# Kernel tuning notes

Hardware: AMD Instinct MI355X
Metric: run time of the kernel (lower is better)

Reference implementation:

```python
import jax, jax.numpy as jnp
import numpy as np

NUM_HEADS = 8
EPS = 1e-6


def _edge_boost(x, density_weight):
    # x: [B, C, H, W] -> boost: [B, H*W] (per-query additive bias)
    B, C, H, W = x.shape
    sx = jnp.array([[-1., 0., 1.], [-2., 0., 2.], [-1., 0., 1.]], dtype=x.dtype)
    sy = jnp.array([[-1., -2., -1.], [0., 0., 0.], [1., 2., 1.]], dtype=x.dtype)
    feat_mean = x.mean(axis=1, keepdims=True)            # [B,1,H,W]
    kern = jnp.stack([sx, sy])[:, None]                  # [2,1,3,3] (OIHW)
    g = jax.lax.conv_general_dilated(
        feat_mean, kern, window_strides=(1, 1), padding='SAME',
        dimension_numbers=('NCHW', 'OIHW', 'NCHW'))     # [B,2,H,W]
    edge = jnp.sqrt(g[:, 0] ** 2 + g[:, 1] ** 2 + EPS)   # [B,H,W]
    return density_weight * jnp.log1p(edge.reshape(B, H * W))


def setup_inputs() -> dict:
    key = jax.random.key(0)
    k1, k2, k3 = jax.random.split(key, 3)
    B, C, H, W = 2, 256, 56, 56
    x = jax.random.normal(k1, (B, C, H, W), dtype=jnp.float32)
    Wqkv = jax.random.normal(k2, (3 * C, C), dtype=jnp.float32) * 0.02
    Wproj = jax.random.normal(k3, (C, C), dtype=jnp.float32) * 0.02
    bproj = jnp.zeros((C,), dtype=jnp.float32)
    density_weight = jnp.float32(1.0)
    return {"x": x, "Wqkv": Wqkv, "Wproj": Wproj, "bproj": bproj,
            "density_weight": density_weight}


def reference(x, Wqkv, Wproj, bproj, density_weight):
    B, C, H, W = x.shape
    h = NUM_HEADS
    d = C // h
    N = H * W
    scale = d ** -0.5

    x_flat = x.reshape(B, C, N).transpose(0, 2, 1)        # [B,N,C]
    qkv = x_flat @ Wqkv.T                                 # [B,N,3C]
    qkv = qkv.reshape(B, N, 3, h, d).transpose(2, 0, 3, 1, 4)  # [3,B,h,N,d]
    q, k, v = qkv[0], qkv[1], qkv[2]

    attn = jnp.einsum('bhqd,bhkd->bhqk', q, k) * scale    # [B,h,N,N]
    boost = _edge_boost(x, density_weight)                # [B,N]
    attn = attn + boost[:, None, :, None]                 # per-query bias, bcast over heads/keys
    attn = jax.nn.softmax(attn, axis=-1)
    # dropout is identity in eval mode

    out = jnp.einsum('bhqk,bhkd->bhqd', attn, v)          # [B,h,N,d]
    out = out.transpose(0, 2, 1, 3).reshape(B, N, C)      # [B,N,C]
    out = out @ Wproj.T + bproj
    return out.transpose(0, 2, 1).reshape(B, C, H, W)
```

## Files before the change

kernel.cpp:

```cpp
#include <hip/hip_runtime.h>
#include <hip/hip_bf16.h>
#include <math.h>

#define NQ    3136
#define CDIM  256
#define HEADS 8
#define NT    49


typedef __attribute__((ext_vector_type(8))) short short8;
typedef __attribute__((ext_vector_type(4))) float f32x4;

__device__ __forceinline__ short f2bf(float f) {
    union { float f; unsigned u; } v; v.f = f;
    unsigned r = v.u + 0x7fff + ((v.u >> 16) & 1);
    return (short)(r >> 16);
}

__device__ __forceinline__ unsigned pk_bf16(float a, float b) {
    unsigned r;
    asm("v_cvt_pk_bf16_f32 %0, %1, %2" : "=v"(r) : "v"(a), "v"(b));
    return r;
}

#define SCALE_L2E 0.25503487523f

__global__ __launch_bounds__(256) void prep(const float* __restrict__ x,
                                            const float* __restrict__ Wq,
                                            const float* __restrict__ Wp,
                                            short* __restrict__ xT,
                                            short* __restrict__ Wb,
                                            short* __restrict__ Wpb) {
    const int bx = blockIdx.x;
    const int t  = threadIdx.x;
    if (bx == 52) {
        const int wp   = blockIdx.y + 4 * blockIdx.z;
        const int base = wp * 8192 + t * 4;
        #pragma unroll
        for (int i = 0; i < 8; ++i) {
            float4 v = *(const float4*)(Wp + base + i * 1024);
            uint2 o = { pk_bf16(v.x, v.y), pk_bf16(v.z, v.w) };
            *(uint2*)(Wpb + base + i * 1024) = o;
        }
        return;
    }
    if (bx >= 49) {
        const int wb   = (bx - 49) + 3 * (blockIdx.y + 4 * blockIdx.z);
        const int base = wb * 8192 + t * 4;
        #pragma unroll
        for (int i = 0; i < 8; ++i) {
            float4 v = *(const float4*)(Wq + base + i * 1024);
            uint2 o = { pk_bf16(v.x, v.y), pk_bf16(v.z, v.w) };
            *(uint2*)(Wb + base + i * 1024) = o;
        }
        return;
    }
    __shared__ short lt[64][72];
    const int b = blockIdx.z, cb = blockIdx.y, nb = bx;
    const float* xb = x + (size_t)b * CDIM * NQ + (size_t)(cb * 64) * NQ + nb * 64;
    #pragma unroll
    for (int it = 0; it < 4; ++it) {
        const int cc = (t >> 4) + 16 * it;
        const int nn = (t & 15) * 4;
        float4 v = *(const float4*)(xb + (size_t)cc * NQ + nn);
        lt[nn + 0][cc] = f2bf(v.x);
        lt[nn + 1][cc] = f2bf(v.y);
        lt[nn + 2][cc] = f2bf(v.z);
        lt[nn + 3][cc] = f2bf(v.w);
    }
    __syncthreads();
    const int n2 = t >> 2, c2 = (t & 3) * 16;
    short* dst = xT + ((size_t)b * NQ + nb * 64 + n2) * CDIM + cb * 64 + c2;
    *(uint4*)dst       = *(const uint4*)&lt[n2][c2];
    *(uint4*)(dst + 8) = *(const uint4*)&lt[n2][c2 + 8];
}

__global__ __launch_bounds__(256) void qkv_mfma(const short* __restrict__ xT,
                                                const short* __restrict__ Wb,
                                                short* __restrict__ Qs,
                                                short* __restrict__ Kb,
                                                short* __restrict__ Vt) {
    __shared__ short xs[64][40];
    __shared__ short wsm[64][40];
    __shared__ short eps[64][72];
    const int nb = blockIdx.x, jb = blockIdx.y, b = blockIdx.z;
    const int n0 = nb * 64, j0 = jb * 64;
    const int t = threadIdx.x;
    const int lane = t & 63, w = t >> 6, g = lane >> 4, ql = lane & 15;
    const int srow = t >> 2, sc = (t & 3) * 8;

    const short* xsrc = xT + ((size_t)b * NQ + n0 + srow) * CDIM + sc;
    const short* wsrc = Wb + (size_t)(j0 + srow) * CDIM + sc;

    short8 xr = *(const short8*)(xsrc);
    short8 wr = *(const short8*)(wsrc);

    f32x4 acc[4] = {};
    for (int c0 = 0; c0 < 256; c0 += 32) {
        *(short8*)&xs[srow][sc]  = xr;
        *(short8*)&wsm[srow][sc] = wr;
        __syncthreads();
        if (c0 + 32 < 256) {
            xr = *(const short8*)(xsrc + c0 + 32);
            wr = *(const short8*)(wsrc + c0 + 32);
        }
        short8 bf = *(const short8*)&wsm[16 * w + ql][8 * g];
        #pragma unroll
        for (int r = 0; r < 4; ++r) {
            short8 af = *(const short8*)&xs[16 * r + ql][8 * g];
            acc[r] = __builtin_amdgcn_mfma_f32_16x16x32_bf16(af, bf, acc[r], 0, 0, 0);
        }
        __syncthreads();
    }

    const int sect = jb >> 2;
    const int hb   = (jb & 3) * 2;
    const int jloc = 16 * w + ql;

    if (sect < 2) {
        const float sc2 = (sect == 0) ? SCALE_L2E : 1.0f;
        #pragma unroll
        for (int r = 0; r < 4; ++r)
            #pragma unroll
            for (int i = 0; i < 4; ++i)
                eps[16 * r + 4 * g + i][jloc] = f2bf(acc[r][i] * sc2);
        __syncthreads();
        short* dstb = (sect == 0) ? Qs : Kb;
        const int n2 = t >> 2, jc = (t & 3) * 16;
        const int head = hb + (jc >> 5), d0 = jc & 31;
        short* dst = dstb + ((size_t)(b * 8 + head) * NQ + n0 + n2) * 32 + d0;
        *(uint4*)dst       = *(const uint4*)&eps[n2][jc];
        *(uint4*)(dst + 8) = *(const uint4*)&eps[n2][jc + 8];
    } else {
        #pragma unroll
        for (int r = 0; r < 4; ++r)
            #pragma unroll
            for (int i = 0; i < 4; ++i)
                eps[jloc][16 * r + 4 * g + i] = f2bf(acc[r][i]);
        __syncthreads();
        const int jl = t >> 2, nc = (t & 3) * 16;
        short* dst = Vt + ((size_t)(b * 8 + hb + (jl >> 5)) * 32 + (jl & 31)) * NQ + n0 + nc;
        *(uint4*)dst       = *(const uint4*)&eps[jl][nc];
        *(uint4*)(dst + 8) = *(const uint4*)&eps[jl][nc + 8];
    }
}

__global__ __launch_bounds__(256) void attn_mfma(const short* __restrict__ Qs,
                                                 const short* __restrict__ Kb,
                                                 const short* __restrict__ Vt,
                                                 short* __restrict__ Ob) {
    __shared__ __align__(16) short vts[2][2][32][72];
    __shared__ __align__(16) short pq[4][32][72];

    const int bid = blockIdx.x;
    const int xcd = bid & 7;
    const int ii  = bid >> 3;
    const int bh  = xcd * 2 + (ii & 1);
    const int q0  = (ii >> 1) * 64;

    const int t    = threadIdx.x;
    const int lane = t & 63;
    const int w    = t >> 6;
    const int g    = lane >> 4;
    const int ql   = lane & 15;
    const int qg   = w & 1, half = w >> 1;
    const int qbase = q0 + 32 * qg;

    const short* Qh = Qs + (size_t)bh * NQ * 32;
    const short* Kh = Kb + (size_t)bh * NQ * 32;
    const short* Vh = Vt + (size_t)bh * 32 * NQ;

    const short8 qfA = *(const short8*)(Qh + (size_t)(qbase + ql) * 32 + 8 * g);
    const short8 qfB = *(const short8*)(Qh + (size_t)(qbase + 16 + ql) * 32 + 8 * g);

    const short* kp = Kh + (size_t)ql * 32 + 8 * g;

    const int vrow = (t & 127) >> 2;
    const int vu   = (t & 3) * 16;

    float lA = 0.f, lB = 0.f;
    f32x4 otA0 = {0,0,0,0}, otA1 = {0,0,0,0};
    f32x4 otB0 = {0,0,0,0}, otB1 = {0,0,0,0};

    short8 vr0 = *(const short8*)(Vh + (size_t)vrow * NQ + half * 64 + vu);
    short8 vr1 = *(const short8*)(Vh + (size_t)vrow * NQ + half * 64 + vu + 8);
    short8 kf0 = *(const short8*)(kp + (size_t)(half * 64 +  0) * 32);
    short8 kf1 = *(const short8*)(kp + (size_t)(half * 64 + 16) * 32);
    short8 kf2 = *(const short8*)(kp + (size_t)(half * 64 + 32) * 32);
    short8 kf3 = *(const short8*)(kp + (size_t)(half * 64 + 48) * 32);
    *(short8*)&vts[half][0][vrow][vu]     = vr0;
    *(short8*)&vts[half][0][vrow][vu + 8] = vr1;
    __syncthreads();

    int buf = 0;
    for (int i = 0; i < 25; ++i) {
        const int cur = 2 * i + half;
        const int nxt = cur + 2;
        if (nxt < NT) {
            vr0 = *(const short8*)(Vh + (size_t)vrow * NQ + nxt * 64 + vu);
            vr1 = *(const short8*)(Vh + (size_t)vrow * NQ + nxt * 64 + vu + 8);
        }

        if (cur < NT) {
            f32x4 stA[4], stB[4];
            stA[0] = __builtin_amdgcn_mfma_f32_16x16x32_bf16(kf0, qfA, (f32x4){0,0,0,0}, 0, 0, 0);
            stB[0] = __builtin_amdgcn_mfma_f32_16x16x32_bf16(kf0, qfB, (f32x4){0,0,0,0}, 0, 0, 0);
            stA[1] = __builtin_amdgcn_mfma_f32_16x16x32_bf16(kf1, qfA, (f32x4){0,0,0,0}, 0, 0, 0);
            stB[1] = __builtin_amdgcn_mfma_f32_16x16x32_bf16(kf1, qfB, (f32x4){0,0,0,0}, 0, 0, 0);
            stA[2] = __builtin_amdgcn_mfma_f32_16x16x32_bf16(kf2, qfA, (f32x4){0,0,0,0}, 0, 0, 0);
            stB[2] = __builtin_amdgcn_mfma_f32_16x16x32_bf16(kf2, qfB, (f32x4){0,0,0,0}, 0, 0, 0);
            stA[3] = __builtin_amdgcn_mfma_f32_16x16x32_bf16(kf3, qfA, (f32x4){0,0,0,0}, 0, 0, 0);
            stB[3] = __builtin_amdgcn_mfma_f32_16x16x32_bf16(kf3, qfB, (f32x4){0,0,0,0}, 0, 0, 0);

            if (nxt < NT) {
                const int kn = nxt * 64;
                kf0 = *(const short8*)(kp + (size_t)(kn +  0) * 32);
                kf1 = *(const short8*)(kp + (size_t)(kn + 16) * 32);
                kf2 = *(const short8*)(kp + (size_t)(kn + 32) * 32);
                kf3 = *(const short8*)(kp + (size_t)(kn + 48) * 32);
            }

            float pA[16], pB[16];
            #pragma unroll
            for (int c = 0; c < 4; ++c)
                #pragma unroll
                for (int e = 0; e < 4; ++e) {
                    pA[4 * c + e] = __builtin_amdgcn_exp2f(stA[c][e]);
                    pB[4 * c + e] = __builtin_amdgcn_exp2f(stB[c][e]);
                }
            float sA = 0.f, sB = 0.f;
            #pragma unroll
            for (int e = 0; e < 16; ++e) { sA += pA[e]; sB += pB[e]; }
            lA += sA; lB += sB;

            #pragma unroll
            for (int c = 0; c < 4; ++c) {
                uint2 va_ = { pk_bf16(pA[4 * c + 0], pA[4 * c + 1]),
                              pk_bf16(pA[4 * c + 2], pA[4 * c + 3]) };
                *(uint2*)&pq[w][ql][16 * c + 4 * g] = va_;
                uint2 vb_ = { pk_bf16(pB[4 * c + 0], pB[4 * c + 1]),
                              pk_bf16(pB[4 * c + 2], pB[4 * c + 3]) };
                *(uint2*)&pq[w][16 + ql][16 * c + 4 * g] = vb_;
            }
            asm volatile("s_waitcnt lgkmcnt(0)" ::: "memory");

            short8 pbA0 = *(const short8*)&pq[w][ql][8 * g];
            short8 pbA1 = *(const short8*)&pq[w][ql][32 + 8 * g];
            short8 pbB0 = *(const short8*)&pq[w][16 + ql][8 * g];
            short8 pbB1 = *(const short8*)&pq[w][16 + ql][32 + 8 * g];
            short8 va00 = *(const short8*)&vts[half][buf][ql][8 * g];
            short8 va01 = *(const short8*)&vts[half][buf][ql][32 + 8 * g];
            short8 va10 = *(const short8*)&vts[half][buf][16 + ql][8 * g];
            short8 va11 = *(const short8*)&vts[half][buf][16 + ql][32 + 8 * g];

            otA0 = __builtin_amdgcn_mfma_f32_16x16x32_bf16(va00, pbA0, otA0, 0, 0, 0);
            otA0 = __builtin_amdgcn_mfma_f32_16x16x32_bf16(va01, pbA1, otA0, 0, 0, 0);
            otA1 = __builtin_amdgcn_mfma_f32_16x16x32_bf16(va10, pbA0, otA1, 0, 0, 0);
            otA1 = __builtin_amdgcn_mfma_f32_16x16x32_bf16(va11, pbA1, otA1, 0, 0, 0);
            otB0 = __builtin_amdgcn_mfma_f32_16x16x32_bf16(va00, pbB0, otB0, 0, 0, 0);
            otB0 = __builtin_amdgcn_mfma_f32_16x16x32_bf16(va01, pbB1, otB0, 0, 0, 0);
            otB1 = __builtin_amdgcn_mfma_f32_16x16x32_bf16(va10, pbB0, otB1, 0, 0, 0);
            otB1 = __builtin_amdgcn_mfma_f32_16x16x32_bf16(va11, pbB1, otB1, 0, 0, 0);
        }

        if (nxt < NT) {
            *(short8*)&vts[half][buf ^ 1][vrow][vu]     = vr0;
            *(short8*)&vts[half][buf ^ 1][vrow][vu + 8] = vr1;
        }
        __syncthreads();
        buf ^= 1;
    }

    lA += __shfl_xor(lA, 16); lA += __shfl_xor(lA, 32);
    lB += __shfl_xor(lB, 16); lB += __shfl_xor(lB, 32);

    float* mrg = (float*)&pq[0][0][0];
    if (half == 1) {
        float* pp = mrg + ((size_t)qg * 64 + lane) * 20;
        *(f32x4*)(pp + 0)  = otA0;
        *(f32x4*)(pp + 4)  = otA1;
        *(f32x4*)(pp + 8)  = otB0;
        *(f32x4*)(pp + 12) = otB1;
        pp[16] = lA; pp[17] = lB;
    }
    __syncthreads();
    if (half == 0) {
        const float* pp = mrg + ((size_t)qg * 64 + lane) * 20;
        f32x4 a0 = *(const f32x4*)(pp + 0);
        f32x4 a1 = *(const f32x4*)(pp + 4);
        f32x4 b0 = *(const f32x4*)(pp + 8);
        f32x4 b1 = *(const f32x4*)(pp + 12);
        const float invA = 1.f / (lA + pp[16]);
        const float invB = 1.f / (lB + pp[17]);
        const int b = bh >> 3, h = bh & 7;
        short* orowA = Ob + ((size_t)b * NQ + qbase + ql) * CDIM + h * 32;
        short* orowB = Ob + ((size_t)b * NQ + qbase + 16 + ql) * CDIM + h * 32;
        uint2 wA0 = { pk_bf16((otA0[0]+a0[0])*invA, (otA0[1]+a0[1])*invA),
                      pk_bf16((otA0[2]+a0[2])*invA, (otA0[3]+a0[3])*invA) };
        uint2 wA1 = { pk_bf16((otA1[0]+a1[0])*invA, (otA1[1]+a1[1])*invA),
                      pk_bf16((otA1[2]+a1[2])*invA, (otA1[3]+a1[3])*invA) };
        uint2 wB0 = { pk_bf16((otB0[0]+b0[0])*invB, (otB0[1]+b0[1])*invB),
                      pk_bf16((otB0[2]+b0[2])*invB, (otB0[3]+b0[3])*invB) };
        uint2 wB1 = { pk_bf16((otB1[0]+b1[0])*invB, (otB1[1]+b1[1])*invB),
                      pk_bf16((otB1[2]+b1[2])*invB, (otB1[3]+b1[3])*invB) };
        *(uint2*)(orowA + 4 * g)      = wA0;
        *(uint2*)(orowA + 16 + 4 * g) = wA1;
        *(uint2*)(orowB + 4 * g)      = wB0;
        *(uint2*)(orowB + 16 + 4 * g) = wB1;
    }
}

__global__ __launch_bounds__(256) void proj_mfma(const short* __restrict__ Ob,
                                                 const short* __restrict__ Wpb,
                                                 const float* __restrict__ bias,
                                                 float* __restrict__ out) {
    __shared__ short xs[32][40];
    __shared__ short wsm[64][40];
    __shared__ float eps[64][36];
    const int n0  = blockIdx.x * 32;
    const int co0 = blockIdx.y * 64;
    const int b   = blockIdx.z;
    const int t   = threadIdx.x;
    const int lane = t & 63, w = t >> 6, g = lane >> 4, ql = lane & 15;
    const int arow = (t & 127) >> 2, ac = (t & 3) * 8;
    const int brow = t >> 2,          bc = (t & 3) * 8;

    const short* asrc = Ob + ((size_t)b * NQ + n0 + arow) * CDIM + ac;
    const short* wsrc = Wpb + (size_t)(co0 + brow) * CDIM + bc;

    short8 ar = {};
    if (t < 128) ar = *(const short8*)(asrc);
    short8 wr = *(const short8*)(wsrc);

    f32x4 acc0 = {}, acc1 = {};
    for (int c0 = 0; c0 < 256; c0 += 32) {
        if (t < 128) *(short8*)&xs[arow][ac] = ar;
        *(short8*)&wsm[brow][bc] = wr;
        __syncthreads();
        if (c0 + 32 < 256) {
            if (t < 128) ar = *(const short8*)(asrc + c0 + 32);
            wr = *(const short8*)(wsrc + c0 + 32);
        }
        short8 bfr = *(const short8*)&wsm[16 * w + ql][8 * g];
        short8 af0 = *(const short8*)&xs[ql][8 * g];
        short8 af1 = *(const short8*)&xs[16 + ql][8 * g];
        acc0 = __builtin_amdgcn_mfma_f32_16x16x32_bf16(af0, bfr, acc0, 0, 0, 0);
        acc1 = __builtin_amdgcn_mfma_f32_16x16x32_bf16(af1, bfr, acc1, 0, 0, 0);
        __syncthreads();
    }

    const int jl = 16 * w + ql;
    const float bb = bias[co0 + jl];
    *(float4*)&eps[jl][4 * g]      = make_float4(acc0[0] + bb, acc0[1] + bb,
                                                 acc0[2] + bb, acc0[3] + bb);
    *(float4*)&eps[jl][16 + 4 * g] = make_float4(acc1[0] + bb, acc1[1] + bb,
                                                 acc1[2] + bb, acc1[3] + bb);
    __syncthreads();

    const int row = t >> 2, seg = (t & 3) * 8;
    float* outp = out + ((size_t)b * CDIM + co0 + row) * NQ + n0 + seg;
    *(float4*)(outp)     = *(const float4*)&eps[row][seg];
    *(float4*)(outp + 4) = *(const float4*)&eps[row][seg + 4];
}

extern "C" void kernel_launch(void* const* d_in, const int* in_sizes, int n_in,
                              void* d_out, int out_size, void* d_ws, size_t ws_size,
                              hipStream_t stream) {
    const float* x     = (const float*)d_in[0];
    const float* Wqkv  = (const float*)d_in[1];
    const float* Wproj = (const float*)d_in[2];
    const float* bproj = (const float*)d_in[3];
    float* out = (float*)d_out;

    short* xT  = (short*)d_ws;
    short* Wb  = xT + (size_t)2 * NQ * CDIM;
    short* Wpb = Wb + (size_t)768 * CDIM;
    short* Qs  = Wpb + (size_t)CDIM * CDIM;
    short* Kb  = Qs + (size_t)16 * NQ * 32;
    short* Vt  = Kb + (size_t)16 * NQ * 32;
    short* Ob  = Vt + (size_t)16 * NQ * 32;

    prep<<<dim3(53, 4, 2), 256, 0, stream>>>(x, Wqkv, Wproj, xT, Wb, Wpb);
    qkv_mfma<<<dim3(49, 12, 2), 256, 0, stream>>>(xT, Wb, Qs, Kb, Vt);
    attn_mfma<<<dim3(784, 1, 1), 256, 0, stream>>>(Qs, Kb, Vt, Ob);
    proj_mfma<<<dim3(98, 4, 2), 256, 0, stream>>>(Ob, Wpb, bproj, out);
}
```

Measured before the change: 78.10 us.

## Halve attention query tile per block and load K fragments in-loop

Each attention block now handles 32 queries instead of 64, with each wave computing one 16-query group, and the grid doubles to 1568 blocks. K fragments are loaded at the top of each iteration instead of being prefetched one step ahead. This cuts per-wave registers and LDS, which can raise occupancy and parallelism. The cost is halved K/V reuse per block, so global K/V traffic doubles, and K load latency is no longer hidden.

```diff
diff --git a/kernel.cpp b/kernel.cpp
--- a/kernel.cpp
+++ b/kernel.cpp
@@ -150,13 +150,13 @@
                                                  const short* __restrict__ Vt,
                                                  short* __restrict__ Ob) {
     __shared__ __align__(16) short vts[2][2][32][72];
-    __shared__ __align__(16) short pq[4][32][72];
+    __shared__ __align__(16) short pq[4][16][72];
 
     const int bid = blockIdx.x;
     const int xcd = bid & 7;
     const int ii  = bid >> 3;
     const int bh  = xcd * 2 + (ii & 1);
-    const int q0  = (ii >> 1) * 64;
+    const int q0  = (ii >> 1) * 32;
 
     const int t    = threadIdx.x;
     const int lane = t & 63;
@@ -164,30 +164,24 @@
     const int g    = lane >> 4;
     const int ql   = lane & 15;
     const int qg   = w & 1, half = w >> 1;
-    const int qbase = q0 + 32 * qg;
+    const int qbase = q0 + 16 * qg;
 
     const short* Qh = Qs + (size_t)bh * NQ * 32;
     const short* Kh = Kb + (size_t)bh * NQ * 32;
     const short* Vh = Vt + (size_t)bh * 32 * NQ;
 
-    const short8 qfA = *(const short8*)(Qh + (size_t)(qbase + ql) * 32 + 8 * g);
-    const short8 qfB = *(const short8*)(Qh + (size_t)(qbase + 16 + ql) * 32 + 8 * g);
+    const short8 qf = *(const short8*)(Qh + (size_t)(qbase + ql) * 32 + 8 * g);
 
     const short* kp = Kh + (size_t)ql * 32 + 8 * g;
 
     const int vrow = (t & 127) >> 2;
     const int vu   = (t & 3) * 16;
 
-    float lA = 0.f, lB = 0.f;
-    f32x4 otA0 = {0,0,0,0}, otA1 = {0,0,0,0};
-    f32x4 otB0 = {0,0,0,0}, otB1 = {0,0,0,0};
+    float l = 0.f;
+    f32x4 ot0 = {0,0,0,0}, ot1 = {0,0,0,0};
 
     short8 vr0 = *(const short8*)(Vh + (size_t)vrow * NQ + half * 64 + vu);
     short8 vr1 = *(const short8*)(Vh + (size_t)vrow * NQ + half * 64 + vu + 8);
-    short8 kf0 = *(const short8*)(kp + (size_t)(half * 64 +  0) * 32);
-    short8 kf1 = *(const short8*)(kp + (size_t)(half * 64 + 16) * 32);
-    short8 kf2 = *(const short8*)(kp + (size_t)(half * 64 + 32) * 32);
-    short8 kf3 = *(const short8*)(kp + (size_t)(half * 64 + 48) * 32);
     *(short8*)&vts[half][0][vrow][vu]     = vr0;
     *(short8*)&vts[half][0][vrow][vu + 8] = vr1;
     __syncthreads();
@@ -202,65 +196,48 @@
         }
 
         if (cur < NT) {
-            f32x4 stA[4], stB[4];
-            stA[0] = __builtin_amdgcn_mfma_f32_16x16x32_bf16(kf0, qfA, (f32x4){0,0,0,0}, 0, 0, 0);
-            stB[0] = __builtin_amdgcn_mfma_f32_16x16x32_bf16(kf0, qfB, (f32x4){0,0,0,0}, 0, 0, 0);
-            stA[1] = __builtin_amdgcn_mfma_f32_16x16x32_bf16(kf1, qfA, (f32x4){0,0,0,0}, 0, 0, 0);
-            stB[1] = __builtin_amdgcn_mfma_f32_16x16x32_bf16(kf1, qfB, (f32x4){0,0,0,0}, 0, 0, 0);
-            stA[2] = __builtin_amdgcn_mfma_f32_16x16x32_bf16(kf2, qfA, (f32x4){0,0,0,0}, 0, 0, 0);
-            stB[2] = __builtin_amdgcn_mfma_f32_16x16x32_bf16(kf2, qfB, (f32x4){0,0,0,0}, 0, 0, 0);
-            stA[3] = __builtin_amdgcn_mfma_f32_16x16x32_bf16(kf3, qfA, (f32x4){0,0,0,0}, 0, 0, 0);
-            stB[3] = __builtin_amdgcn_mfma_f32_16x16x32_bf16(kf3, qfB, (f32x4){0,0,0,0}, 0, 0, 0);
-
-            if (nxt < NT) {
-                const int kn = nxt * 64;
-                kf0 = *(const short8*)(kp + (size_t)(kn +  0) * 32);
-                kf1 = *(const short8*)(kp + (size_t)(kn + 16) * 32);
-                kf2 = *(const short8*)(kp + (size_t)(kn + 32) * 32);
-                kf3 = *(const short8*)(kp + (size_t)(kn + 48) * 32);
-            }
-
-            float pA[16], pB[16];
+            const int k0 = cur * 64;
+            short8 kf0 = *(const short8*)(kp + (size_t)(k0 +  0) * 32);
+            short8 kf1 = *(const short8*)(kp + (size_t)(k0 + 16) * 32);
+            short8 kf2 = *(const short8*)(kp + (size_t)(k0 + 32) * 32);
+            short8 kf3 = *(const short8*)(kp + (size_t)(k0 + 48) * 32);
+
+            f32x4 st[4];
+            st[0] = __builtin_amdgcn_mfma_f32_16x16x32_bf16(kf0, qf, (f32x4){0,0,0,0}, 0, 0, 0);
+            st[1] = __builtin_amdgcn_mfma_f32_16x16x32_bf16(kf1, qf, (f32x4){0,0,0,0}, 0, 0, 0);
+            st[2] = __builtin_amdgcn_mfma_f32_16x16x32_bf16(kf2, qf, (f32x4){0,0,0,0}, 0, 0, 0);
+            st[3] = __builtin_amdgcn_mfma_f32_16x16x32_bf16(kf3, qf, (f32x4){0,0,0,0}, 0, 0, 0);
+
+            float p[16];
             #pragma unroll
             for (int c = 0; c < 4; ++c)
                 #pragma unroll
-                for (int e = 0; e < 4; ++e) {
-                    pA[4 * c + e] = __builtin_amdgcn_exp2f(stA[c][e]);
-                    pB[4 * c + e] = __builtin_amdgcn_exp2f(stB[c][e]);
-                }
-            float sA = 0.f, sB = 0.f;
-            #pragma unroll
-            for (int e = 0; e < 16; ++e) { sA += pA[e]; sB += pB[e]; }
-            lA += sA; lB += sB;
+                for (int e = 0; e < 4; ++e)
+                    p[4 * c + e] = __builtin_amdgcn_exp2f(st[c][e]);
+            float s = 0.f;
+            #pragma unroll
+            for (int e = 0; e < 16; ++e) s += p[e];
+            l += s;
 
             #pragma unroll
             for (int c = 0; c < 4; ++c) {
-                uint2 va_ = { pk_bf16(pA[4 * c + 0], pA[4 * c + 1]),
-                              pk_bf16(pA[4 * c + 2], pA[4 * c + 3]) };
-                *(uint2*)&pq[w][ql][16 * c + 4 * g] = va_;
-                uint2 vb_ = { pk_bf16(pB[4 * c + 0], pB[4 * c + 1]),
-                              pk_bf16(pB[4 * c + 2], pB[4 * c + 3]) };
-                *(uint2*)&pq[w][16 + ql][16 * c + 4 * g] = vb_;
+                uint2 pv = { pk_bf16(p[4 * c + 0], p[4 * c + 1]),
+                             pk_bf16(p[4 * c + 2], p[4 * c + 3]) };
+                *(uint2*)&pq[w][ql][16 * c + 4 * g] = pv;
             }
             asm volatile("s_waitcnt lgkmcnt(0)" ::: "memory");
 
-            short8 pbA0 = *(const short8*)&pq[w][ql][8 * g];
-            short8 pbA1 = *(const short8*)&pq[w][ql][32 + 8 * g];
-            short8 pbB0 = *(const short8*)&pq[w][16 + ql][8 * g];
-            short8 pbB1 = *(const short8*)&pq[w][16 + ql][32 + 8 * g];
+            short8 pb0  = *(const short8*)&pq[w][ql][8 * g];
+            short8 pb1  = *(const short8*)&pq[w][ql][32 + 8 * g];
             short8 va00 = *(const short8*)&vts[half][buf][ql][8 * g];
             short8 va01 = *(const short8*)&vts[half][buf][ql][32 + 8 * g];
             short8 va10 = *(const short8*)&vts[half][buf][16 + ql][8 * g];
             short8 va11 = *(const short8*)&vts[half][buf][16 + ql][32 + 8 * g];
 
-            otA0 = __builtin_amdgcn_mfma_f32_16x16x32_bf16(va00, pbA0, otA0, 0, 0, 0);
-            otA0 = __builtin_amdgcn_mfma_f32_16x16x32_bf16(va01, pbA1, otA0, 0, 0, 0);
-            otA1 = __builtin_amdgcn_mfma_f32_16x16x32_bf16(va10, pbA0, otA1, 0, 0, 0);
-            otA1 = __builtin_amdgcn_mfma_f32_16x16x32_bf16(va11, pbA1, otA1, 0, 0, 0);
-            otB0 = __builtin_amdgcn_mfma_f32_16x16x32_bf16(va00, pbB0, otB0, 0, 0, 0);
-            otB0 = __builtin_amdgcn_mfma_f32_16x16x32_bf16(va01, pbB1, otB0, 0, 0, 0);
-            otB1 = __builtin_amdgcn_mfma_f32_16x16x32_bf16(va10, pbB0, otB1, 0, 0, 0);
-            otB1 = __builtin_amdgcn_mfma_f32_16x16x32_bf16(va11, pbB1, otB1, 0, 0, 0);
+            ot0 = __builtin_amdgcn_mfma_f32_16x16x32_bf16(va00, pb0, ot0, 0, 0, 0);
+            ot0 = __builtin_amdgcn_mfma_f32_16x16x32_bf16(va01, pb1, ot0, 0, 0, 0);
+            ot1 = __builtin_amdgcn_mfma_f32_16x16x32_bf16(va10, pb0, ot1, 0, 0, 0);
+            ot1 = __builtin_amdgcn_mfma_f32_16x16x32_bf16(va11, pb1, ot1, 0, 0, 0);
         }
 
         if (nxt < NT) {
@@ -271,42 +248,30 @@
         buf ^= 1;
     }
 
-    lA += __shfl_xor(lA, 16); lA += __shfl_xor(lA, 32);
-    lB += __shfl_xor(lB, 16); lB += __shfl_xor(lB, 32);
+    l += __shfl_xor(l, 16);
+    l += __shfl_xor(l, 32);
 
     float* mrg = (float*)&pq[0][0][0];
     if (half == 1) {
-        float* pp = mrg + ((size_t)qg * 64 + lane) * 20;
-        *(f32x4*)(pp + 0)  = otA0;
-        *(f32x4*)(pp + 4)  = otA1;
-        *(f32x4*)(pp + 8)  = otB0;
-        *(f32x4*)(pp + 12) = otB1;
-        pp[16] = lA; pp[17] = lB;
+        float* pp = mrg + ((size_t)qg * 64 + lane) * 12;
+        *(f32x4*)(pp + 0) = ot0;
+        *(f32x4*)(pp + 4) = ot1;
+        pp[8] = l;
     }
     __syncthreads();
     if (half == 0) {
-        const float* pp = mrg + ((size_t)qg * 64 + lane) * 20;
+        const float* pp = mrg + ((size_t)qg * 64 + lane) * 12;
         f32x4 a0 = *(const f32x4*)(pp + 0);
         f32x4 a1 = *(const f32x4*)(pp + 4);
-        f32x4 b0 = *(const f32x4*)(pp + 8);
-        f32x4 b1 = *(const f32x4*)(pp + 12);
-        const float invA = 1.f / (lA + pp[16]);
-        const float invB = 1.f / (lB + pp[17]);
+        const float inv = 1.f / (l + pp[8]);
         const int b = bh >> 3, h = bh & 7;
-        short* orowA = Ob + ((size_t)b * NQ + qbase + ql) * CDIM + h * 32;
-        short* orowB = Ob + ((size_t)b * NQ + qbase + 16 + ql) * CDIM + h * 32;
-        uint2 wA0 = { pk_bf16((otA0[0]+a0[0])*invA, (otA0[1]+a0[1])*invA),
-                      pk_bf16((otA0[2]+a0[2])*invA, (otA0[3]+a0[3])*invA) };
-        uint2 wA1 = { pk_bf16((otA1[0]+a1[0])*invA, (otA1[1]+a1[1])*invA),
-                      pk_bf16((otA1[2]+a1[2])*invA, (otA1[3]+a1[3])*invA) };
-        uint2 wB0 = { pk_bf16((otB0[0]+b0[0])*invB, (otB0[1]+b0[1])*invB),
-                      pk_bf16((otB0[2]+b0[2])*invB, (otB0[3]+b0[3])*invB) };
-        uint2 wB1 = { pk_bf16((otB1[0]+b1[0])*invB, (otB1[1]+b1[1])*invB),
-                      pk_bf16((otB1[2]+b1[2])*invB, (otB1[3]+b1[3])*invB) };
-        *(uint2*)(orowA + 4 * g)      = wA0;
-        *(uint2*)(orowA + 16 + 4 * g) = wA1;
-        *(uint2*)(orowB + 4 * g)      = wB0;
-        *(uint2*)(orowB + 16 + 4 * g) = wB1;
+        short* orow = Ob + ((size_t)b * NQ + qbase + ql) * CDIM + h * 32;
+        uint2 w0 = { pk_bf16((ot0[0]+a0[0])*inv, (ot0[1]+a0[1])*inv),
+                     pk_bf16((ot0[2]+a0[2])*inv, (ot0[3]+a0[3])*inv) };
+        uint2 w1 = { pk_bf16((ot1[0]+a1[0])*inv, (ot1[1]+a1[1])*inv),
+                     pk_bf16((ot1[2]+a1[2])*inv, (ot1[3]+a1[3])*inv) };
+        *(uint2*)(orow + 4 * g)      = w0;
+        *(uint2*)(orow + 16 + 4 * g) = w1;
     }
 }
 
@@ -382,6 +347,6 @@
 
     prep<<<dim3(53, 4, 2), 256, 0, stream>>>(x, Wqkv, Wproj, xT, Wb, Wpb);
     qkv_mfma<<<dim3(49, 12, 2), 256, 0, stream>>>(xT, Wb, Qs, Kb, Vt);
-    attn_mfma<<<dim3(784, 1, 1), 256, 0, stream>>>(Qs, Kb, Vt, Ob);
+    attn_mfma<<<dim3(1568, 1, 1), 256, 0, stream>>>(Qs, Kb, Vt, Ob);
     proj_mfma<<<dim3(98, 4, 2), 256, 0, stream>>>(Ob, Wpb, bproj, out);
 }
```

After: 88.46 us. 1.13x slower.

## Compute softmax row sums via MFMA with ones vector, add setprio, drop K prefetch

Applied to the files above, without the earlier changes.

Replaces the scalar VALU accumulation and cross-lane shuffle reduction of the softmax denominator with extra MFMA ops that multiply the bf16 probabilities by a ones vector. It also wraps the MFMA groups in s_setprio to favour matrix issue across waves. K fragments are now loaded at the start of each tile instead of being prefetched one tile ahead. The sum now uses the bf16-rounded probabilities, which matches the numerator, but adds four MFMAs per tile and exposes K load latency.

```diff
diff --git a/kernel.cpp b/kernel.cpp
--- a/kernel.cpp
+++ b/kernel.cpp
@@ -173,21 +173,21 @@
     const short8 qfA = *(const short8*)(Qh + (size_t)(qbase + ql) * 32 + 8 * g);
     const short8 qfB = *(const short8*)(Qh + (size_t)(qbase + 16 + ql) * 32 + 8 * g);
 
+    short8 ones;
+    #pragma unroll
+    for (int e = 0; e < 8; ++e) ones[e] = (short)0x3F80;
+
     const short* kp = Kh + (size_t)ql * 32 + 8 * g;
 
     const int vrow = (t & 127) >> 2;
     const int vu   = (t & 3) * 16;
 
-    float lA = 0.f, lB = 0.f;
     f32x4 otA0 = {0,0,0,0}, otA1 = {0,0,0,0};
     f32x4 otB0 = {0,0,0,0}, otB1 = {0,0,0,0};
+    f32x4 otlA = {0,0,0,0}, otlB = {0,0,0,0};
 
     short8 vr0 = *(const short8*)(Vh + (size_t)vrow * NQ + half * 64 + vu);
     short8 vr1 = *(const short8*)(Vh + (size_t)vrow * NQ + half * 64 + vu + 8);
-    short8 kf0 = *(const short8*)(kp + (size_t)(half * 64 +  0) * 32);
-    short8 kf1 = *(const short8*)(kp + (size_t)(half * 64 + 16) * 32);
-    short8 kf2 = *(const short8*)(kp + (size_t)(half * 64 + 32) * 32);
-    short8 kf3 = *(const short8*)(kp + (size_t)(half * 64 + 48) * 32);
     *(short8*)&vts[half][0][vrow][vu]     = vr0;
     *(short8*)&vts[half][0][vrow][vu + 8] = vr1;
     __syncthreads();
@@ -202,6 +202,13 @@
         }
 
         if (cur < NT) {
+            const int k0 = cur * 64;
+            short8 kf0 = *(const short8*)(kp + (size_t)(k0 +  0) * 32);
+            short8 kf1 = *(const short8*)(kp + (size_t)(k0 + 16) * 32);
+            short8 kf2 = *(const short8*)(kp + (size_t)(k0 + 32) * 32);
+            short8 kf3 = *(const short8*)(kp + (size_t)(k0 + 48) * 32);
+
+            __builtin_amdgcn_s_setprio(1);
             f32x4 stA[4], stB[4];
             stA[0] = __builtin_amdgcn_mfma_f32_16x16x32_bf16(kf0, qfA, (f32x4){0,0,0,0}, 0, 0, 0);
             stB[0] = __builtin_amdgcn_mfma_f32_16x16x32_bf16(kf0, qfB, (f32x4){0,0,0,0}, 0, 0, 0);
@@ -211,14 +218,7 @@
             stB[2] = __builtin_amdgcn_mfma_f32_16x16x32_bf16(kf2, qfB, (f32x4){0,0,0,0}, 0, 0, 0);
             stA[3] = __builtin_amdgcn_mfma_f32_16x16x32_bf16(kf3, qfA, (f32x4){0,0,0,0}, 0, 0, 0);
             stB[3] = __builtin_amdgcn_mfma_f32_16x16x32_bf16(kf3, qfB, (f32x4){0,0,0,0}, 0, 0, 0);
-
-            if (nxt < NT) {
-                const int kn = nxt * 64;
-                kf0 = *(const short8*)(kp + (size_t)(kn +  0) * 32);
-                kf1 = *(const short8*)(kp + (size_t)(kn + 16) * 32);
-                kf2 = *(const short8*)(kp + (size_t)(kn + 32) * 32);
-                kf3 = *(const short8*)(kp + (size_t)(kn + 48) * 32);
-            }
+            __builtin_amdgcn_s_setprio(0);
 
             float pA[16], pB[16];
             #pragma unroll
@@ -228,10 +228,6 @@
                     pA[4 * c + e] = __builtin_amdgcn_exp2f(stA[c][e]);
                     pB[4 * c + e] = __builtin_amdgcn_exp2f(stB[c][e]);
                 }
-            float sA = 0.f, sB = 0.f;
-            #pragma unroll
-            for (int e = 0; e < 16; ++e) { sA += pA[e]; sB += pB[e]; }
-            lA += sA; lB += sB;
 
             #pragma unroll
             for (int c = 0; c < 4; ++c) {
@@ -253,6 +249,7 @@
             short8 va10 = *(const short8*)&vts[half][buf][16 + ql][8 * g];
             short8 va11 = *(const short8*)&vts[half][buf][16 + ql][32 + 8 * g];
 
+            __builtin_amdgcn_s_setprio(1);
             otA0 = __builtin_amdgcn_mfma_f32_16x16x32_bf16(va00, pbA0, otA0, 0, 0, 0);
             otA0 = __builtin_amdgcn_mfma_f32_16x16x32_bf16(va01, pbA1, otA0, 0, 0, 0);
             otA1 = __builtin_amdgcn_mfma_f32_16x16x32_bf16(va10, pbA0, otA1, 0, 0, 0);
@@ -261,6 +258,11 @@
             otB0 = __builtin_amdgcn_mfma_f32_16x16x32_bf16(va01, pbB1, otB0, 0, 0, 0);
             otB1 = __builtin_amdgcn_mfma_f32_16x16x32_bf16(va10, pbB0, otB1, 0, 0, 0);
             otB1 = __builtin_amdgcn_mfma_f32_16x16x32_bf16(va11, pbB1, otB1, 0, 0, 0);
+            otlA = __builtin_amdgcn_mfma_f32_16x16x32_bf16(ones, pbA0, otlA, 0, 0, 0);
+            otlA = __builtin_amdgcn_mfma_f32_16x16x32_bf16(ones, pbA1, otlA, 0, 0, 0);
+            otlB = __builtin_amdgcn_mfma_f32_16x16x32_bf16(ones, pbB0, otlB, 0, 0, 0);
+            otlB = __builtin_amdgcn_mfma_f32_16x16x32_bf16(ones, pbB1, otlB, 0, 0, 0);
+            __builtin_amdgcn_s_setprio(0);
         }
 
         if (nxt < NT) {
@@ -271,8 +273,8 @@
         buf ^= 1;
     }
 
-    lA += __shfl_xor(lA, 16); lA += __shfl_xor(lA, 32);
-    lB += __shfl_xor(lB, 16); lB += __shfl_xor(lB, 32);
+    const float lA = otlA[0];
+    const float lB = otlB[0];
 
     float* mrg = (float*)&pq[0][0][0];
     if (half == 1) {
```

Result: faster. 69.40 us (-11.1%).
